# Kernel optimization log

Hardware: AMD Instinct MI355X
Metric: run time of the kernel (lower is better)

## Reference

```python
import jax, jax.numpy as jnp
import numpy as np

B = 1; H = 192; W = 192; DIM = 128; HEADS = 8
WS = 16                      # window_size
OWS = 24                     # overlap_win_size = int(16*0.5)+16
PAD = 4                      # (OWS-WS)//2
C2 = DIM // 2                # per-branch channels
H2 = HEADS // 2              # per-branch heads
HID = 256                    # mlp_ratio * dim
TBL = (WS + OWS - 1) ** 2    # 1521 rel-pos table entries
SCALE = (C2 // H2) ** (-0.5) # head_dim ** -0.5


def layer_norm(x, w, b, eps=1e-5):
    mu = jnp.mean(x, -1, keepdims=True)
    var = jnp.mean((x - mu) ** 2, -1, keepdims=True)
    return (x - mu) * jax.lax.rsqrt(var + eps) * w + b


def window_partition(x, ws):
    b, h, w, c = x.shape
    x = x.reshape(b, h // ws, ws, w // ws, ws, c).transpose(0, 1, 3, 2, 4, 5)
    return x.reshape(-1, ws, ws, c)


def window_reverse(win, ws, h, w):
    b = win.shape[0] // ((h // ws) * (w // ws))
    x = win.reshape(b, h // ws, w // ws, ws, ws, -1).transpose(0, 1, 3, 2, 4, 5)
    return x.reshape(b, h, w, -1)


def _patch_idx(h, w):
    ri = (jnp.arange(h // WS) * WS)[:, None] + jnp.arange(OWS)  # (nwh, OWS)
    ci = (jnp.arange(w // WS) * WS)[:, None] + jnp.arange(OWS)  # (nww, OWS)
    return ri, ci


def unfold_patches(x):
    # x: (b, h, w, c) -> (b*nw, OWS*OWS, c); matches nn.Unfold(OWS, stride=WS, pad=PAD)
    b, h, w, c = x.shape
    xp = jnp.pad(x, ((0, 0), (PAD, PAD), (PAD, PAD), (0, 0)))
    ri, ci = _patch_idx(h, w)
    p = xp[:, ri[:, None, :, None], ci[None, :, None, :], :]  # (b,nwh,nww,OWS,OWS,c)
    return p.reshape(-1, OWS * OWS, c)


def fold_patches(p, b, h, w):
    # inverse of unfold: scatter-add overlapping patches into (b, h+2PAD, w+2PAD, c)
    nwh, nww = h // WS, w // WS
    c = p.shape[-1]
    p = p.reshape(b, nwh, nww, OWS, OWS, c)
    ri, ci = _patch_idx(h, w)
    canvas = jnp.zeros((b, h + 2 * PAD, w + 2 * PAD, c), p.dtype)
    return canvas.at[:, ri[:, None, :, None], ci[None, :, None, :], :].add(p)


def cubic_kernel(x, A=-0.75):
    # PyTorch bicubic (cubic convolution, A=-0.75)
    ax = jnp.abs(x)
    w1 = ((A + 2.0) * ax - (A + 3.0)) * ax * ax + 1.0
    w2 = A * (ax * (ax * (ax - 5.0) + 8.0) - 4.0)
    return jnp.where(ax <= 1.0, w1, jnp.where(ax < 2.0, w2, 0.0))


def resize_matrix(n_out, n_in):
    # dense 1-D bicubic resize matrix, align_corners=False, border-clamped (torch semantics)
    i = jnp.arange(n_out, dtype=jnp.float32)
    src = (i + 0.5) * (float(n_in) / float(n_out)) - 0.5
    fl = jnp.floor(src)
    idx = fl[:, None] + jnp.arange(-1, 3, dtype=jnp.float32)[None, :]  # (n_out, 4)
    wts = cubic_kernel(src[:, None] - idx)
    idx_c = jnp.clip(idx, 0, n_in - 1).astype(jnp.int32)
    M = jnp.zeros((n_out, n_in), jnp.float32)
    return M.at[jnp.arange(n_out)[:, None], idx_c].add(wts)


def cross_attn(xq, xkv, rpi, wq, wkv, rpb):
    b_, nq, d = xq.shape
    n = xkv.shape[1]
    q = (xq @ wq).reshape(b_, nq, H2, -1).transpose(0, 2, 1, 3)
    k, v = jnp.split(xkv @ wkv, 2, axis=-1)
    k = k.reshape(b_, n, H2, -1).transpose(0, 2, 1, 3)
    v = v.reshape(b_, n, H2, -1).transpose(0, 2, 1, 3)
    attn = jnp.einsum('bhqd,bhkd->bhqk', q * SCALE, k)
    bias = rpb[rpi.reshape(-1)].reshape(WS * WS, OWS * OWS, H2)
    bias = bias.transpose(2, 0, 1) if nq < n else bias.transpose(2, 1, 0)
    attn = jax.nn.softmax(attn + bias[None], axis=-1)
    out = jnp.einsum('bhqk,bhkd->bhqd', attn, v)
    return out.transpose(0, 2, 1, 3).reshape(b_, nq, d)


def gsfn(x, h, w, fc1_w, fc1_b, sgn_w, sgn_b, conv_w, conv_b, fc2_w, fc2_b):
    x = x @ fc1_w + fc1_b  # NOTE: source GSFN never applies self.act
    x1, x2 = jnp.split(x, 2, axis=-1)
    Bn, N, Ch = x2.shape
    x2 = layer_norm(x2, sgn_w, sgn_b).transpose(0, 2, 1).reshape(Bn, Ch, h, w)
    x2 = jax.lax.conv_general_dilated(
        x2, conv_w, (1, 1), ((1, 1), (1, 1)),
        feature_group_count=Ch, dimension_numbers=('NCHW', 'OIHW', 'NCHW'))
    x2 = x2 + conv_b[None, :, None, None]
    x2 = x2.reshape(Bn, Ch, N).transpose(0, 2, 1)
    return (x1 * x2) @ fc2_w + fc2_b


def mstb(x_tkn, ln1_w, ln1_b, q1_w, kv1_w, rpb1, q2_w, kv2_w, rpb2,
         proj_w, proj_b, ln2_w, ln2_b, fc1_w, fc1_b, sgn_w, sgn_b,
         conv_w, conv_b, fc2_w, fc2_b, rpi, h, w):
    b, _, c = x_tkn.shape
    short = x_tkn
    x = layer_norm(x_tkn, ln1_w, ln1_b).reshape(b, h, w, c)
    xw = window_partition(x, WS).reshape(-1, WS * WS, c)     # (b*nw, ws*ws, c)
    xa, xb = jnp.split(xw, 2, axis=-1)
    xb_img = window_reverse(xb.reshape(-1, WS, WS, C2), WS, h, w)  # (b,h,w,C2)
    xb_p = unfold_patches(xb_img)                            # (b*nw, OWS*OWS, C2)
    a = cross_attn(xa, xb_p, rpi, q1_w, kv1_w, rpb1) + xa
    bb = cross_attn(xb_p, xa, rpi, q2_w, kv2_w, rpb2) + xb_p
    folded = fold_patches(bb, b, h, w)                       # (b, h+2p, w+2p, C2)
    Mh = resize_matrix(h, h + 2 * PAD)
    Mw = resize_matrix(w, w + 2 * PAD)
    resized = jnp.einsum('oi,bijc,pj->bopc', Mh, folded, Mw)  # bicubic to (h,w)
    xb2 = window_partition(resized, WS).reshape(-1, WS * WS, C2)
    x = jnp.concatenate([a, xb2], -1)
    x = window_reverse(x.reshape(-1, WS, WS, c), WS, h, w).reshape(b, h * w, c)
    x = x @ proj_w + proj_b + short
    x = gsfn(layer_norm(x, ln2_w, ln2_b), h, w, fc1_w, fc1_b,
             sgn_w, sgn_b, conv_w, conv_b, fc2_w, fc2_b) + x
    return x


def setup_inputs() -> dict:
    key = jax.random.key(0)
    ks = jax.random.split(key, 12)
    rn = lambda k, s, sc: jax.random.normal(k, s, jnp.float32) * sc
    return {
        'x_tkn': jax.random.normal(ks[0], (B, H * W, DIM), jnp.float32),
        'ln1_w': jnp.ones((DIM,), jnp.float32), 'ln1_b': jnp.zeros((DIM,), jnp.float32),
        'q1_w': rn(ks[1], (C2, C2), 0.05), 'kv1_w': rn(ks[2], (C2, 2 * C2), 0.05),
        'rpb1': rn(ks[3], (TBL, H2), 0.02),
        'q2_w': rn(ks[4], (C2, C2), 0.05), 'kv2_w': rn(ks[5], (C2, 2 * C2), 0.05),
        'rpb2': rn(ks[6], (TBL, H2), 0.02),
        'proj_w': rn(ks[7], (DIM, DIM), 0.05), 'proj_b': jnp.zeros((DIM,), jnp.float32),
        'ln2_w': jnp.ones((DIM,), jnp.float32), 'ln2_b': jnp.zeros((DIM,), jnp.float32),
        'fc1_w': rn(ks[8], (DIM, HID), 0.05), 'fc1_b': jnp.zeros((HID,), jnp.float32),
        'sgn_w': jnp.ones((HID // 2,), jnp.float32), 'sgn_b': jnp.zeros((HID // 2,), jnp.float32),
        'conv_w': rn(ks[9], (HID // 2, 1, 3, 3), 0.1), 'conv_b': jnp.zeros((HID // 2,), jnp.float32),
        'fc2_w': rn(ks[10], (HID // 2, DIM), 0.05), 'fc2_b': jnp.zeros((DIM,), jnp.float32),
        'rpi': jax.random.randint(ks[11], (WS * WS, OWS * OWS), 0, TBL),
        'h': H, 'w': W,
    }


def reference(x_tkn, ln1_w, ln1_b, q1_w, kv1_w, rpb1, q2_w, kv2_w, rpb2,
              proj_w, proj_b, ln2_w, ln2_b, fc1_w, fc1_b, sgn_w, sgn_b,
              conv_w, conv_b, fc2_w, fc2_b, rpi, h, w):
    return mstb(x_tkn, ln1_w, ln1_b, q1_w, kv1_w, rpb1, q2_w, kv2_w, rpb2,
                proj_w, proj_b, ln2_w, ln2_b, fc1_w, fc1_b, sgn_w, sgn_b,
                conv_w, conv_b, fc2_w, fc2_b, rpi, h, w)
```

## Files before the change

kernel.cpp:

```cpp
#include <hip/hip_runtime.h>
#include <hip/hip_bf16.h>

#define HH 192
#define WW 192
#define NWIN 12
#define WSZ 16
#define OWSZ 24
#define PADK 4
#define NQ1 256
#define NKV1 576
#define C2K 64
#define H2K 4
#define HD 16
#define NTOK (HH*WW)
#define LOG2E 1.4426950408889634f
#define QSCALE (0.25f * LOG2E)

typedef __hip_bfloat16 bf16;
typedef __attribute__((ext_vector_type(8))) short bf16x8;
typedef __attribute__((ext_vector_type(4))) float f32x4;

union B8 { short s[8]; bf16x8 v; unsigned u[4]; };

__device__ __forceinline__ unsigned cvtpk(float lo, float hi)
{
    unsigned r;
    asm("v_cvt_pk_bf16_f32 %0, %1, %2" : "=v"(r) : "v"(lo), "v"(hi));
    return r;
}

__launch_bounds__(256)
__global__ void ln_kernel(const float* __restrict__ in, int is, int io,
                          float* __restrict__ out, int os, int oo,
                          const float* __restrict__ g, const float* __restrict__ b,
                          int M)
{
    int row = blockIdx.x * 4 + (threadIdx.x >> 6);
    if (row >= M) return;
    int lane = threadIdx.x & 63;
    const float* p = in + (size_t)row * is + io;
    float v0 = p[lane * 2], v1 = p[lane * 2 + 1];
    float s = v0 + v1, sq = v0 * v0 + v1 * v1;
#pragma unroll
    for (int o = 32; o > 0; o >>= 1) { s += __shfl_xor(s, o); sq += __shfl_xor(sq, o); }
    float mu  = s * 0.0078125f;
    float var = sq * 0.0078125f - mu * mu;
    float inv = 1.0f / sqrtf(var + 1e-5f);
    float* q = out + (size_t)row * os + oo;
    q[lane * 2]     = (v0 - mu) * inv * g[lane * 2]     + b[lane * 2];
    q[lane * 2 + 1] = (v1 - mu) * inv * g[lane * 2 + 1] + b[lane * 2 + 1];
}

__global__ void wcombT_kernel(const float* __restrict__ q1_w, const float* __restrict__ kv1_w,
                              const float* __restrict__ q2_w, const float* __restrict__ kv2_w,
                              bf16* __restrict__ WT)
{
    int idx = blockIdx.x * 256 + threadIdx.x;
    if (idx >= 384 * 128) return;
    int c = idx >> 7, r = idx & 127;
    float v = 0.f;
    if (c < 64)       { if (r < 64)  v = q1_w[r * 64 + c] * QSCALE; }
    else if (c < 192) { if (r >= 64) v = kv1_w[(r - 64) * 128 + (c - 64)]; }
    else if (c < 256) { if (r >= 64) v = q2_w[(r - 64) * 64 + (c - 192)] * QSCALE; }
    else              { if (r < 64)  v = kv2_w[r * 128 + (c - 256)]; }
    WT[idx] = __float2bfloat16(v);
}

__global__ void wtrans_kernel(const float* __restrict__ src, int N, bf16* __restrict__ dst)
{
// ... 5 lines not shown

__global__ void bias1_kernel(const float* __restrict__ rpb1, const int* __restrict__ rpi,
                             float* __restrict__ biasT)
{
    int idx = blockIdx.x * 256 + threadIdx.x;
    if (idx >= H2K * NKV1 * NQ1) return;
    int q = idx & 255;
    int n = (idx >> 8) % NKV1;
    int h = idx / (NKV1 * NQ1);
    biasT[idx] = rpb1[rpi[q * NKV1 + n] * H2K + h] * LOG2E;
}

__global__ void bias2_kernel(const float* __restrict__ rpb2, const int* __restrict__ rpi,
                             float* __restrict__ biasT)
{
    int idx = blockIdx.x * 256 + threadIdx.x;
    if (idx >= H2K * NQ1 * NKV1) return;
    int q = idx % NKV1;
    int k = (idx / NKV1) % NQ1;
    int h = idx / (NKV1 * NQ1);
    biasT[idx] = rpb2[rpi[k * NKV1 + q] * H2K + h] * LOG2E;
}

__launch_bounds__(256)
__global__ void attn1_mfma(const unsigned* __restrict__ qkvu,
                           const float* __restrict__ lnx,
                           const float* __restrict__ biasT,
                           float* __restrict__ xcat)
{
    __shared__ unsigned K_lds[NKV1][10];
    __shared__ unsigned V_lds[NKV1][10];

    const int win = blockIdx.x, h = blockIdx.y;
    const int wi = win / NWIN, wj = win % NWIN;
    const int tid = threadIdx.x;
    const int lane = tid & 63, w = tid >> 6;
    const int g = lane >> 4, qloc = lane & 15;

    for (int n = tid; n < NKV1; n += 256) {
        int rr = wi * WSZ - PADK + n / OWSZ, cc = wj * WSZ - PADK + n % OWSZ;
        bool ib = (rr >= 0 && rr < HH && cc >= 0 && cc < WW);
        uint4 k0v = make_uint4(0, 0, 0, 0), k1v = k0v, v0v = k0v, v1v = k0v;
        if (ib) {
            const unsigned* src = qkvu + (size_t)(rr * WW + cc) * 96 + 32 + 8 * h;
            k0v = *(const uint4*)(src);
            k1v = *(const uint4*)(src + 4);
            v0v = *(const uint4*)(src + 32);
            v1v = *(const uint4*)(src + 36);
        }
        *(uint4*)&K_lds[n][0] = k0v; *(uint4*)&K_lds[n][4] = k1v;
        *(uint4*)&V_lds[n][0] = v0v; *(uint4*)&V_lds[n][4] = v1v;
    }
    __syncthreads();

    const int q0base = blockIdx.z * 128 + w * 32;
    bf16x8 qfrag[2];
#pragma unroll
    for (int qt = 0; qt < 2; qt++) {
        int q = q0base + qt * 16 + qloc;
        int pix = (wi * WSZ + (q >> 4)) * WW + wj * WSZ + (q & 15);
        B8 f;
#pragma unroll
        for (int j = 0; j < 4; j++) f.u[j] = 0;
        if (g < 2)
            f.v = *(const bf16x8*)(qkvu + (size_t)pix * 96 + 8 * h + 4 * g);
        qfrag[qt] = f.v;
    }

    f32x4 O[2];
    float lsum[2];
#pragma unroll
    for (int qt = 0; qt < 2; qt++) { O[qt] = (f32x4){0.f, 0.f, 0.f, 0.f}; lsum[qt] = 0.f; }
    const f32x4 zz = {0.f, 0.f, 0.f, 0.f};

    for (int step = 0; step < 18; step++) {
        const int k0 = step * 32;
        bf16x8 kfA, kfB;
        if (g < 2) {
            kfA = *(const bf16x8*)&K_lds[k0 + qloc][4 * g];
            kfB = *(const bf16x8*)&K_lds[k0 + 16 + qloc][4 * g];
        } else {
            B8 zf;
#pragma unroll
            for (int j = 0; j < 4; j++) zf.u[j] = 0;
            kfA = zf.v; kfB = zf.v;
        }
        B8 vf;
#pragma unroll
        for (int j = 0; j < 8; j++) {
            int key = k0 + 4 * g + (j & 3) + ((j >> 2) << 4);
            unsigned word = V_lds[key][qloc >> 1];
            vf.s[j] = (short)((qloc & 1) ? (word >> 16) : (word & 0xffff));
        }

#pragma unroll
        for (int qt = 0; qt < 2; qt++) {
            f32x4 sA = __builtin_amdgcn_mfma_f32_16x16x32_bf16(kfA, qfrag[qt], zz, 0, 0, 0);
            f32x4 sB = __builtin_amdgcn_mfma_f32_16x16x32_bf16(kfB, qfrag[qt], zz, 0, 0, 0);
            int qa = q0base + qt * 16 + qloc;
            const float* bpA = biasT + ((size_t)h * NKV1 + k0 + 4 * g) * NQ1 + qa;
            const float* bpB = bpA + 16 * NQ1;
            float pa[4], pb[4];
            float ls = 0.f;
#pragma unroll
            for (int r = 0; r < 4; r++) {
                pa[r] = exp2f(sA[r] + bpA[(size_t)r * NQ1]);
                pb[r] = exp2f(sB[r] + bpB[(size_t)r * NQ1]);
                ls += pa[r] + pb[r];
            }
            B8 pf;
            pf.u[0] = cvtpk(pa[0], pa[1]);
            pf.u[1] = cvtpk(pa[2], pa[3]);
            pf.u[2] = cvtpk(pb[0], pb[1]);
            pf.u[3] = cvtpk(pb[2], pb[3]);
            lsum[qt] += ls;
            O[qt] = __builtin_amdgcn_mfma_f32_16x16x32_bf16(vf.v, pf.v, O[qt], 0, 0, 0);
        }
    }

#pragma unroll
    for (int qt = 0; qt < 2; qt++) {
        float lt = lsum[qt];
        lt += __shfl_xor(lt, 16);
        lt += __shfl_xor(lt, 32);
        float rl = 1.f / lt;
        int q = q0base + qt * 16 + qloc;
        int pix = (wi * WSZ + (q >> 4)) * WW + wj * WSZ + (q & 15);
        size_t base = (size_t)pix * 128 + h * HD + 4 * g;
#pragma unroll
        for (int r = 0; r < 4; r++)
            xcat[base + r] = O[qt][r] * rl + lnx[base + r];
    }
}

__launch_bounds__(256)
__global__ void attn2_mfma(const unsigned* __restrict__ qkvu,
                           const float* __restrict__ lnx,
                           const float* __restrict__ biasT,
                           float* __restrict__ bb)
{
    __shared__ unsigned K_lds[NQ1][10];
    __shared__ unsigned V_lds[NQ1][10];

    const int win = blockIdx.x, h = blockIdx.y;
    const int wi = win / NWIN, wj = win % NWIN;
    const int tid = threadIdx.x;
    const int lane = tid & 63, w = tid >> 6;
    const int g = lane >> 4, qloc = lane & 15;

    {
        int n = tid;
        int pix = (wi * WSZ + (n >> 4)) * WW + wj * WSZ + (n & 15);
        const unsigned* src = qkvu + (size_t)pix * 96 + 32 + 8 * h;
        *(uint4*)&K_lds[n][0] = *(const uint4*)(src);
        *(uint4*)&K_lds[n][4] = *(const uint4*)(src + 4);
        *(uint4*)&V_lds[n][0] = *(const uint4*)(src + 32);
        *(uint4*)&V_lds[n][4] = *(const uint4*)(src + 36);
    }
    __syncthreads();

    const int q0base = blockIdx.z * 192 + w * 48;
    bf16x8 qfrag[3];
    bool qin[3];
    int qpix[3];
#pragma unroll
    for (int qt = 0; qt < 3; qt++) {
        int qa = q0base + qt * 16 + qloc;
        int gr = wi * WSZ - PADK + qa / OWSZ, gc = wj * WSZ - PADK + qa % OWSZ;
        bool ib = (gr >= 0 && gr < HH && gc >= 0 && gc < WW);
        qin[qt] = ib;
        qpix[qt] = ib ? gr * WW + gc : 0;
        B8 f;
#pragma unroll
        for (int j = 0; j < 4; j++) f.u[j] = 0;
        if (ib && g < 2)
            f.v = *(const bf16x8*)(qkvu + (size_t)qpix[qt] * 96 + 8 * h + 4 * g);
        qfrag[qt] = f.v;
    }

    f32x4 O[3];
    float lsum[3];
#pragma unroll
    for (int qt = 0; qt < 3; qt++) { O[qt] = (f32x4){0.f, 0.f, 0.f, 0.f}; lsum[qt] = 0.f; }
    const f32x4 zz = {0.f, 0.f, 0.f, 0.f};

    for (int step = 0; step < 8; step++) {
        const int k0 = step * 32;
        bf16x8 kfA, kfB;
        if (g < 2) {
            kfA = *(const bf16x8*)&K_lds[k0 + qloc][4 * g];
            kfB = *(const bf16x8*)&K_lds[k0 + 16 + qloc][4 * g];
        } else {
            B8 zf;
#pragma unroll
            for (int j = 0; j < 4; j++) zf.u[j] = 0;
            kfA = zf.v; kfB = zf.v;
        }
        B8 vf;
#pragma unroll
        for (int j = 0; j < 8; j++) {
            int key = k0 + 4 * g + (j & 3) + ((j >> 2) << 4);
            unsigned word = V_lds[key][qloc >> 1];
            vf.s[j] = (short)((qloc & 1) ? (word >> 16) : (word & 0xffff));
        }

#pragma unroll
        for (int qt = 0; qt < 3; qt++) {
            f32x4 sA = __builtin_amdgcn_mfma_f32_16x16x32_bf16(kfA, qfrag[qt], zz, 0, 0, 0);
            f32x4 sB = __builtin_amdgcn_mfma_f32_16x16x32_bf16(kfB, qfrag[qt], zz, 0, 0, 0);
            int qa = q0base + qt * 16 + qloc;
            const float* bpA = biasT + ((size_t)h * NQ1 + k0 + 4 * g) * NKV1 + qa;
            const float* bpB = bpA + 16 * NKV1;
            float pa[4], pb[4];
            float ls = 0.f;
#pragma unroll
            for (int r = 0; r < 4; r++) {
                pa[r] = exp2f(sA[r] + bpA[(size_t)r * NKV1]);
                pb[r] = exp2f(sB[r] + bpB[(size_t)r * NKV1]);
                ls += pa[r] + pb[r];
            }
            B8 pf;
            pf.u[0] = cvtpk(pa[0], pa[1]);
            pf.u[1] = cvtpk(pa[2], pa[3]);
            pf.u[2] = cvtpk(pb[0], pb[1]);
            pf.u[3] = cvtpk(pb[2], pb[3]);
            lsum[qt] += ls;
            O[qt] = __builtin_amdgcn_mfma_f32_16x16x32_bf16(vf.v, pf.v, O[qt], 0, 0, 0);
        }
    }

#pragma unroll
    for (int qt = 0; qt < 3; qt++) {
        float lt = lsum[qt];
        lt += __shfl_xor(lt, 16);
        lt += __shfl_xor(lt, 32);
        float rl = 1.f / lt;
        int qa = q0base + qt * 16 + qloc;
        size_t obase = ((size_t)win * NKV1 + qa) * C2K + h * HD + 4 * g;
        size_t rbase = (size_t)qpix[qt] * 128 + C2K + h * HD + 4 * g;
#pragma unroll
        for (int r = 0; r < 4; r++)
            bb[obase + r] = O[qt][r] * rl + (qin[qt] ? lnx[rbase + r] : 0.f);
    }
}

__global__ void fold_kernel(const float* __restrict__ bb, float* __restrict__ folded)
{
    int idx = blockIdx.x * 256 + threadIdx.x;
    if (idx >= 200 * 200 * 64) return;
    int c = idx & 63;
    int j = (idx >> 6) % 200;
    int i = idx / (64 * 200);
    int ilo = (i > 23) ? ((i - 8) >> 4) : 0;
    int ihi = min(11, i >> 4);
    int jlo = (j > 23) ? ((j - 8) >> 4) : 0;
    int jhi = min(11, j >> 4);
    float s = 0.f;
    for (int wi = ilo; wi <= ihi; wi++)
        for (int wj = jlo; wj <= jhi; wj++) {
            int p = (i - wi * 16) * OWSZ + (j - wj * 16);
            s += bb[((size_t)(wi * NWIN + wj) * NKV1 + p) * C2K + c];
        }
    folded[idx] = s;
}

__device__ __forceinline__ float cubicw(float x)
{
    float ax = fabsf(x);
    const float A = -0.75f;
    if (ax <= 1.f) return ((A + 2.f) * ax - (A + 3.f)) * ax * ax + 1.f;
    if (ax < 2.f)  return A * (ax * (ax * (ax - 5.f) + 8.f) - 4.f);
    return 0.f;
}

__global__ void resize_kernel(const float* __restrict__ folded, float* __restrict__ xcat)
{
    int idx = blockIdx.x * 256 + threadIdx.x;
    if (idx >= HH * WW * C2K) return;
    int c = idx & 63;
    int p = (idx >> 6) % WW;
    int o = idx / (C2K * WW);
    const float ratio = 200.f / 192.f;
    float sr = (o + 0.5f) * ratio - 0.5f;
    float sc = (p + 0.5f) * ratio - 0.5f;
    int fr = (int)floorf(sr), fcc = (int)floorf(sc);
    float wc[4]; int ic[4];
#pragma unroll
    for (int u = 0; u < 4; u++) {
        int jj = fcc - 1 + u;
        wc[u] = cubicw(sc - (float)jj);
        ic[u] = min(max(jj, 0), 199);
    }
    float acc = 0.f;
#pragma unroll
    for (int t = 0; t < 4; t++) {
        int ii = fr - 1 + t;
        float wr = cubicw(sr - (float)ii);
        int ir = min(max(ii, 0), 199);
        const float* rowp = folded + ((size_t)ir * 200) * 64 + c;
        float rs = 0.f;
#pragma unroll
        for (int u = 0; u < 4; u++) rs += wc[u] * rowp[(size_t)ic[u] * 64];
        acc += wr * rs;
    }
    xcat[(size_t)(o * WW + p) * 128 + C2K + c] = acc;
}

template<int NTPW, bool OBF>
__launch_bounds__(256)
__global__ void gemm_mfma(const float* __restrict__ A1, int a1s,
                          const float* __restrict__ A2, int a2s,
                          const bf16* __restrict__ WT,
                          const float* __restrict__ bias,
                          const float* __restrict__ R, int rs,
                          float* __restrict__ C, int cs)
{
    const int tid = threadIdx.x;
    const int lane = tid & 63, w = tid >> 6;
    const int g = lane >> 4, nl = lane & 15;

    bf16x8 wf[NTPW][4];
#pragma unroll
    for (int t = 0; t < NTPW; t++) {
        int ncol = (w * NTPW + t) * 16 + nl;
        const bf16* wp = WT + (size_t)ncol * 128;
#pragma unroll
        for (int ks = 0; ks < 4; ks++)
            wf[t][ks] = *(const bf16x8*)(wp + ks * 32 + 8 * g);
    }

    const f32x4 zz = {0.f, 0.f, 0.f, 0.f};
    const int row = (blockIdx.x * 4 + blockIdx.y) * 16 + nl;

    bf16x8 xf[4];
    const float* ap = A1 + (size_t)row * a1s + 8 * g;
#pragma unroll
    for (int ks = 0; ks < 4; ks++) {
        float4 v0 = *(const float4*)(ap + ks * 32);
        float4 v1 = *(const float4*)(ap + ks * 32 + 4);
        if (A2) {
            const float* ap2 = A2 + (size_t)row * a2s + 8 * g + ks * 32;
            float4 m0 = *(const float4*)(ap2);
            float4 m1 = *(const float4*)(ap2 + 4);
            v0.x *= m0.x; v0.y *= m0.y; v0.z *= m0.z; v0.w *= m0.w;
            v1.x *= m1.x; v1.y *= m1.y; v1.z *= m1.z; v1.w *= m1.w;
        }
        B8 f;
        f.u[0] = cvtpk(v0.x, v0.y);
// ... 13 lines not shown
            acc[t] = __builtin_amdgcn_mfma_f32_16x16x32_bf16(wf[t][ks], xf[ks], acc[t], 0, 0, 0);

#pragma unroll
    for (int t = 0; t < NTPW; t++) {
        const int n0t = (w * NTPW + t) * 16 + 4 * g;
        if (OBF) {
            unsigned* Cu = (unsigned*)C + (size_t)row * (cs >> 1) + (n0t >> 1);
            uint2 o;
            o.x = cvtpk(acc[t][0], acc[t][1]);
            o.y = cvtpk(acc[t][2], acc[t][3]);
            *(uint2*)Cu = o;
        } else {
            float4 o;
            o.x = acc[t][0]; o.y = acc[t][1]; o.z = acc[t][2]; o.w = acc[t][3];
            if (bias) {
                float4 bv = *(const float4*)(bias + n0t);
                o.x += bv.x; o.y += bv.y; o.z += bv.z; o.w += bv.w;
            }
            if (R) {
                float4 rv = *(const float4*)(R + (size_t)row * rs + n0t);
                o.x += rv.x; o.y += rv.y; o.z += rv.z; o.w += rv.w;
            }
            *(float4*)(C + (size_t)row * cs + n0t) = o;
        }
    }
}

__global__ void dwconv_kernel(const float* __restrict__ x2n,
                              const float* __restrict__ conv_w,
                              const float* __restrict__ conv_b,
                              float* __restrict__ x2c)
{
    int idx = blockIdx.x * 256 + threadIdx.x;
    if (idx >= NTOK * 128) return;
    int ch = idx & 127, t = idx >> 7;
    int i = t / WW, j = t % WW;
    float acc = conv_b[ch];
#pragma unroll
    for (int a = 0; a < 3; a++) {
        int ii = i + a - 1;
        if (ii < 0 || ii >= HH) continue;
#pragma unroll
        for (int b = 0; b < 3; b++) {
            int jj = j + b - 1;
            if (jj < 0 || jj >= WW) continue;
            acc += conv_w[ch * 9 + a * 3 + b] * x2n[(size_t)(ii * WW + jj) * 256 + ch];
// ... 24 lines not shown
    const float* fc1_b  = (const float*)d_in[14];
    const float* sgn_w  = (const float*)d_in[15];
    const float* sgn_b  = (const float*)d_in[16];
    const float* conv_w = (const float*)d_in[17];
    const float* conv_b = (const float*)d_in[18];
    const float* fc2_w  = (const float*)d_in[19];
    const float* fc2_b  = (const float*)d_in[20];
    const int*   rpi    = (const int*)d_in[21];

    float* ws = (float*)d_ws;
    float* lnx    = ws;
    float* xcat   = ws + 4718592;
    float* bbuf   = ws + 9437184;
    bf16*  projT  = (bf16*)(ws + 14155776);
    bf16*  fc1T   = (bf16*)(ws + 14163968);
    bf16*  fc2T   = (bf16*)(ws + 14180352);
    float* bias1T = ws + 14745600;
    float* bias2T = ws + 17104896;
    float* qkv    = ws + 17694720;
    bf16*  wcombT = (bf16*)(ws + 21233664);
    float* foldp  = ws + 17694720;
    float* h1     = ws + 14745600;
    float* out    = (float*)d_out;

    ln_kernel<<<NTOK / 4, 256, 0, stream>>>(x_tkn, 128, 0, lnx, 128, 0, ln1_w, ln1_b, NTOK);
    wcombT_kernel<<<(384 * 128) / 256, 256, 0, stream>>>(q1_w, kv1_w, q2_w, kv2_w, wcombT);
    bias1_kernel<<<(H2K * NKV1 * NQ1) / 256, 256, 0, stream>>>(rpb1, rpi, bias1T);
    bias2_kernel<<<(H2K * NQ1 * NKV1) / 256, 256, 0, stream>>>(rpb2, rpi, bias2T);
    gemm_mfma<3, true><<<dim3(NTOK / 64, 4), 256, 0, stream>>>(lnx, 128, nullptr, 0, wcombT,
                                                               nullptr, nullptr, 0, qkv, 192);
    attn1_mfma<<<dim3(144, 4, 2), 256, 0, stream>>>((const unsigned*)qkv, lnx, bias1T, xcat);
    gemm_mfma<3, true><<<dim3(NTOK / 64, 4), 256, 0, stream>>>(lnx, 128, nullptr, 0,
                                                               wcombT + 192 * 128,
                                                               nullptr, nullptr, 0, qkv, 192);
    attn2_mfma<<<dim3(144, 4, 3), 256, 0, stream>>>((const unsigned*)qkv, lnx, bias2T, bbuf);
    fold_kernel<<<(200 * 200 * 64) / 256, 256, 0, stream>>>(bbuf, foldp);
    wtrans_kernel<<<(128 * 128) / 256, 256, 0, stream>>>(proj_w, 128, projT);
    wtrans_kernel<<<(256 * 128) / 256, 256, 0, stream>>>(fc1_w, 256, fc1T);
    wtrans_kernel<<<(128 * 128) / 256, 256, 0, stream>>>(fc2_w, 128, fc2T);
    resize_kernel<<<(HH * WW * C2K) / 256, 256, 0, stream>>>(foldp, xcat);
    gemm_mfma<2, false><<<dim3(NTOK / 64, 4), 256, 0, stream>>>(xcat, 128, nullptr, 0, projT,
                                                                proj_b, x_tkn, 128, lnx, 128);
    ln_kernel<<<NTOK / 4, 256, 0, stream>>>(lnx, 128, 0, bbuf, 128, 0, ln2_w, ln2_b, NTOK);
    gemm_mfma<4, false><<<dim3(NTOK / 64, 4), 256, 0, stream>>>(bbuf, 128, nullptr, 0, fc1T,
                                                                fc1_b, nullptr, 0, h1, 256);
    ln_kernel<<<NTOK / 4, 256, 0, stream>>>(h1, 256, 128, h1, 256, 128, sgn_w, sgn_b, NTOK);
    dwconv_kernel<<<(NTOK * 128) / 256, 256, 0, stream>>>(h1 + 128, conv_w, conv_b, xcat);
    gemm_mfma<2, false><<<dim3(NTOK / 64, 4), 256, 0, stream>>>(h1, 256, xcat, 128, fc2T,
                                                                fc2_b, lnx, 128, out, 128);
}
```

Measured before the change: 323.3 us.

## Fuse LayerNorm2 into proj GEMM and SG-norm into fc1 GEMM epilogues

After: 305.1 us. 5.6% less time.

```diff
diff --git a/kernel.cpp b/kernel.cpp
--- a/kernel.cpp
+++ b/kernel.cpp
@@ -44,7 +44,7 @@
 #pragma unroll
     for (int o = 32; o > 0; o >>= 1) { s += __shfl_xor(s, o); sq += __shfl_xor(sq, o); }
     float mu  = s * 0.0078125f;
-    float var = sq * 0.0078125f - mu * mu;
+    float var = fmaxf(sq * 0.0078125f - mu * mu, 0.f);
     float inv = 1.0f / sqrtf(var + 1e-5f);
     float* q = out + (size_t)row * os + oo;
     q[lane * 2]     = (v0 - mu) * inv * g[lane * 2]     + b[lane * 2];
@@ -96,290 +96,6 @@
     biasT[idx] = rpb2[rpi[k * NKV1 + q] * H2K + h] * LOG2E;
 }
 
-__launch_bounds__(256)
-__global__ void attn1_mfma(const unsigned* __restrict__ qkvu,
-                           const float* __restrict__ lnx,
-                           const float* __restrict__ biasT,
-                           float* __restrict__ xcat)
-{
-    __shared__ unsigned K_lds[NKV1][10];
-    __shared__ unsigned V_lds[NKV1][10];
-
-    const int win = blockIdx.x, h = blockIdx.y;
-    const int wi = win / NWIN, wj = win % NWIN;
-    const int tid = threadIdx.x;
-    const int lane = tid & 63, w = tid >> 6;
-    const int g = lane >> 4, qloc = lane & 15;
-
-    for (int n = tid; n < NKV1; n += 256) {
-        int rr = wi * WSZ - PADK + n / OWSZ, cc = wj * WSZ - PADK + n % OWSZ;
-        bool ib = (rr >= 0 && rr < HH && cc >= 0 && cc < WW);
-        uint4 k0v = make_uint4(0, 0, 0, 0), k1v = k0v, v0v = k0v, v1v = k0v;
-        if (ib) {
-            const unsigned* src = qkvu + (size_t)(rr * WW + cc) * 96 + 32 + 8 * h;
-            k0v = *(const uint4*)(src);
-            k1v = *(const uint4*)(src + 4);
-            v0v = *(const uint4*)(src + 32);
-            v1v = *(const uint4*)(src + 36);
-        }
-        *(uint4*)&K_lds[n][0] = k0v; *(uint4*)&K_lds[n][4] = k1v;
-        *(uint4*)&V_lds[n][0] = v0v; *(uint4*)&V_lds[n][4] = v1v;
-    }
-    __syncthreads();
-
-    const int q0base = blockIdx.z * 128 + w * 32;
-    bf16x8 qfrag[2];
-#pragma unroll
-    for (int qt = 0; qt < 2; qt++) {
-        int q = q0base + qt * 16 + qloc;
-        int pix = (wi * WSZ + (q >> 4)) * WW + wj * WSZ + (q & 15);
-        B8 f;
-#pragma unroll
-        for (int j = 0; j < 4; j++) f.u[j] = 0;
-        if (g < 2)
-            f.v = *(const bf16x8*)(qkvu + (size_t)pix * 96 + 8 * h + 4 * g);
-        qfrag[qt] = f.v;
-    }
-
-    f32x4 O[2];
-    float lsum[2];
-#pragma unroll
-    for (int qt = 0; qt < 2; qt++) { O[qt] = (f32x4){0.f, 0.f, 0.f, 0.f}; lsum[qt] = 0.f; }
-    const f32x4 zz = {0.f, 0.f, 0.f, 0.f};
-
-    for (int step = 0; step < 18; step++) {
-        const int k0 = step * 32;
-        bf16x8 kfA, kfB;
-        if (g < 2) {
-            kfA = *(const bf16x8*)&K_lds[k0 + qloc][4 * g];
-            kfB = *(const bf16x8*)&K_lds[k0 + 16 + qloc][4 * g];
-        } else {
-            B8 zf;
-#pragma unroll
-            for (int j = 0; j < 4; j++) zf.u[j] = 0;
-            kfA = zf.v; kfB = zf.v;
-        }
-        B8 vf;
-#pragma unroll
-        for (int j = 0; j < 8; j++) {
-            int key = k0 + 4 * g + (j & 3) + ((j >> 2) << 4);
-            unsigned word = V_lds[key][qloc >> 1];
-            vf.s[j] = (short)((qloc & 1) ? (word >> 16) : (word & 0xffff));
-        }
-
-#pragma unroll
-        for (int qt = 0; qt < 2; qt++) {
-            f32x4 sA = __builtin_amdgcn_mfma_f32_16x16x32_bf16(kfA, qfrag[qt], zz, 0, 0, 0);
-            f32x4 sB = __builtin_amdgcn_mfma_f32_16x16x32_bf16(kfB, qfrag[qt], zz, 0, 0, 0);
-            int qa = q0base + qt * 16 + qloc;
-            const float* bpA = biasT + ((size_t)h * NKV1 + k0 + 4 * g) * NQ1 + qa;
-            const float* bpB = bpA + 16 * NQ1;
-            float pa[4], pb[4];
-            float ls = 0.f;
-#pragma unroll
-            for (int r = 0; r < 4; r++) {
-                pa[r] = exp2f(sA[r] + bpA[(size_t)r * NQ1]);
-                pb[r] = exp2f(sB[r] + bpB[(size_t)r * NQ1]);
-                ls += pa[r] + pb[r];
-            }
-            B8 pf;
-            pf.u[0] = cvtpk(pa[0], pa[1]);
-            pf.u[1] = cvtpk(pa[2], pa[3]);
-            pf.u[2] = cvtpk(pb[0], pb[1]);
-            pf.u[3] = cvtpk(pb[2], pb[3]);
-            lsum[qt] += ls;
-            O[qt] = __builtin_amdgcn_mfma_f32_16x16x32_bf16(vf.v, pf.v, O[qt], 0, 0, 0);
-        }
-    }
-
-#pragma unroll
-    for (int qt = 0; qt < 2; qt++) {
-        float lt = lsum[qt];
-        lt += __shfl_xor(lt, 16);
-        lt += __shfl_xor(lt, 32);
-        float rl = 1.f / lt;
-        int q = q0base + qt * 16 + qloc;
-        int pix = (wi * WSZ + (q >> 4)) * WW + wj * WSZ + (q & 15);
-        size_t base = (size_t)pix * 128 + h * HD + 4 * g;
-#pragma unroll
-        for (int r = 0; r < 4; r++)
-            xcat[base + r] = O[qt][r] * rl + lnx[base + r];
-    }
-}
-
-__launch_bounds__(256)
-__global__ void attn2_mfma(const unsigned* __restrict__ qkvu,
-                           const float* __restrict__ lnx,
-                           const float* __restrict__ biasT,
-                           float* __restrict__ bb)
-{
-    __shared__ unsigned K_lds[NQ1][10];
-    __shared__ unsigned V_lds[NQ1][10];
-
-    const int win = blockIdx.x, h = blockIdx.y;
-    const int wi = win / NWIN, wj = win % NWIN;
-    const int tid = threadIdx.x;
-    const int lane = tid & 63, w = tid >> 6;
-    const int g = lane >> 4, qloc = lane & 15;
-
-    {
-        int n = tid;
-        int pix = (wi * WSZ + (n >> 4)) * WW + wj * WSZ + (n & 15);
-        const unsigned* src = qkvu + (size_t)pix * 96 + 32 + 8 * h;
-        *(uint4*)&K_lds[n][0] = *(const uint4*)(src);
-        *(uint4*)&K_lds[n][4] = *(const uint4*)(src + 4);
-        *(uint4*)&V_lds[n][0] = *(const uint4*)(src + 32);
-        *(uint4*)&V_lds[n][4] = *(const uint4*)(src + 36);
-    }
-    __syncthreads();
-
-    const int q0base = blockIdx.z * 192 + w * 48;
-    bf16x8 qfrag[3];
-    bool qin[3];
-    int qpix[3];
-#pragma unroll
-    for (int qt = 0; qt < 3; qt++) {
-        int qa = q0base + qt * 16 + qloc;
-        int gr = wi * WSZ - PADK + qa / OWSZ, gc = wj * WSZ - PADK + qa % OWSZ;
-        bool ib = (gr >= 0 && gr < HH && gc >= 0 && gc < WW);
-        qin[qt] = ib;
-        qpix[qt] = ib ? gr * WW + gc : 0;
-        B8 f;
-#pragma unroll
-        for (int j = 0; j < 4; j++) f.u[j] = 0;
-        if (ib && g < 2)
-            f.v = *(const bf16x8*)(qkvu + (size_t)qpix[qt] * 96 + 8 * h + 4 * g);
-        qfrag[qt] = f.v;
-    }
-
-    f32x4 O[3];
-    float lsum[3];
-#pragma unroll
-    for (int qt = 0; qt < 3; qt++) { O[qt] = (f32x4){0.f, 0.f, 0.f, 0.f}; lsum[qt] = 0.f; }
-    const f32x4 zz = {0.f, 0.f, 0.f, 0.f};
-
-    for (int step = 0; step < 8; step++) {
-        const int k0 = step * 32;
-        bf16x8 kfA, kfB;
-        if (g < 2) {
-            kfA = *(const bf16x8*)&K_lds[k0 + qloc][4 * g];
-            kfB = *(const bf16x8*)&K_lds[k0 + 16 + qloc][4 * g];
-        } else {
-            B8 zf;
-#pragma unroll
-            for (int j = 0; j < 4; j++) zf.u[j] = 0;
-            kfA = zf.v; kfB = zf.v;
-        }
-        B8 vf;
-#pragma unroll
-        for (int j = 0; j < 8; j++) {
-            int key = k0 + 4 * g + (j & 3) + ((j >> 2) << 4);
-            unsigned word = V_lds[key][qloc >> 1];
-            vf.s[j] = (short)((qloc & 1) ? (word >> 16) : (word & 0xffff));
-        }
-
-#pragma unroll
-        for (int qt = 0; qt < 3; qt++) {
-            f32x4 sA = __builtin_amdgcn_mfma_f32_16x16x32_bf16(kfA, qfrag[qt], zz, 0, 0, 0);
-            f32x4 sB = __builtin_amdgcn_mfma_f32_16x16x32_bf16(kfB, qfrag[qt], zz, 0, 0, 0);
-            int qa = q0base + qt * 16 + qloc;
-            const float* bpA = biasT + ((size_t)h * NQ1 + k0 + 4 * g) * NKV1 + qa;
-            const float* bpB = bpA + 16 * NKV1;
-            float pa[4], pb[4];
-            float ls = 0.f;
-#pragma unroll
-            for (int r = 0; r < 4; r++) {
-                pa[r] = exp2f(sA[r] + bpA[(size_t)r * NKV1]);
-                pb[r] = exp2f(sB[r] + bpB[(size_t)r * NKV1]);
-                ls += pa[r] + pb[r];
-            }
-            B8 pf;
-            pf.u[0] = cvtpk(pa[0], pa[1]);
-            pf.u[1] = cvtpk(pa[2], pa[3]);
-            pf.u[2] = cvtpk(pb[0], pb[1]);
-            pf.u[3] = cvtpk(pb[2], pb[3]);
-            lsum[qt] += ls;
-            O[qt] = __builtin_amdgcn_mfma_f32_16x16x32_bf16(vf.v, pf.v, O[qt], 0, 0, 0);
-        }
-    }
-
-#pragma unroll
-    for (int qt = 0; qt < 3; qt++) {
-        float lt = lsum[qt];
-        lt += __shfl_xor(lt, 16);
-        lt += __shfl_xor(lt, 32);
-        float rl = 1.f / lt;
-        int qa = q0base + qt * 16 + qloc;
-        size_t obase = ((size_t)win * NKV1 + qa) * C2K + h * HD + 4 * g;
-        size_t rbase = (size_t)qpix[qt] * 128 + C2K + h * HD + 4 * g;
-#pragma unroll
-        for (int r = 0; r < 4; r++)
-            bb[obase + r] = O[qt][r] * rl + (qin[qt] ? lnx[rbase + r] : 0.f);
-    }
-}
-
-__global__ void fold_kernel(const float* __restrict__ bb, float* __restrict__ folded)
-{
-    int idx = blockIdx.x * 256 + threadIdx.x;
-    if (idx >= 200 * 200 * 64) return;
-    int c = idx & 63;
-    int j = (idx >> 6) % 200;
-    int i = idx / (64 * 200);
-    int ilo = (i > 23) ? ((i - 8) >> 4) : 0;
-    int ihi = min(11, i >> 4);
-    int jlo = (j > 23) ? ((j - 8) >> 4) : 0;
-    int jhi = min(11, j >> 4);
-    float s = 0.f;
-    for (int wi = ilo; wi <= ihi; wi++)
-        for (int wj = jlo; wj <= jhi; wj++) {
-            int p = (i - wi * 16) * OWSZ + (j - wj * 16);
-            s += bb[((size_t)(wi * NWIN + wj) * NKV1 + p) * C2K + c];
-        }
-    folded[idx] = s;
-}
-
-__device__ __forceinline__ float cubicw(float x)
-{
-    float ax = fabsf(x);
-    const float A = -0.75f;
-    if (ax <= 1.f) return ((A + 2.f) * ax - (A + 3.f)) * ax * ax + 1.f;
-    if (ax < 2.f)  return A * (ax * (ax * (ax - 5.f) + 8.f) - 4.f);
-    return 0.f;
-}
-
-__global__ void resize_kernel(const float* __restrict__ folded, float* __restrict__ xcat)
-{
-    int idx = blockIdx.x * 256 + threadIdx.x;
-    if (idx >= HH * WW * C2K) return;
-    int c = idx & 63;
-    int p = (idx >> 6) % WW;
-    int o = idx / (C2K * WW);
-    const float ratio = 200.f / 192.f;
-    float sr = (o + 0.5f) * ratio - 0.5f;
-    float sc = (p + 0.5f) * ratio - 0.5f;
-    int fr = (int)floorf(sr), fcc = (int)floorf(sc);
-    float wc[4]; int ic[4];
-#pragma unroll
-    for (int u = 0; u < 4; u++) {
-        int jj = fcc - 1 + u;
-        wc[u] = cubicw(sc - (float)jj);
-        ic[u] = min(max(jj, 0), 199);
-    }
-    float acc = 0.f;
-#pragma unroll
-    for (int t = 0; t < 4; t++) {
-        int ii = fr - 1 + t;
-        float wr = cubicw(sr - (float)ii);
-        int ir = min(max(ii, 0), 199);
-        const float* rowp = folded + ((size_t)ir * 200) * 64 + c;
-        float rs = 0.f;
-#pragma unroll
-        for (int u = 0; u < 4; u++) rs += wc[u] * rowp[(size_t)ic[u] * 64];
-        acc += wr * rs;
-    }
-    xcat[(size_t)(o * WW + p) * 128 + C2K + c] = acc;
-}
-
 template<int NTPW, bool OBF>
 __launch_bounds__(256)
 __global__ void gemm_mfma(const float* __restrict__ A1, int a1s,
@@ -396,8 +112,7 @@
     bf16x8 wf[NTPW][4];
 #pragma unroll
     for (int t = 0; t < NTPW; t++) {
-        int ncol = (w * NTPW + t) * 16 + nl;
-        const bf16* wp = WT + (size_t)ncol * 128;
+        const bf16* wp = WT + (size_t)((w * NTPW + t) * 16 + nl) * 128;
 #pragma unroll
         for (int ks = 0; ks < 4; ks++)
             wf[t][ks] = *(const bf16x8*)(wp + ks * 32 + 8 * g);
@@ -457,6 +172,480 @@
                 o.x += rv.x; o.y += rv.y; o.z += rv.z; o.w += rv.w;
             }
             *(float4*)(C + (size_t)row * cs + n0t) = o;
+        }
+    }
+}
+
+__launch_bounds__(256)
+__global__ void attn1_mfma(const unsigned* __restrict__ qkvu,
+                           const float* __restrict__ lnx,
+                           const float* __restrict__ biasT,
+                           float* __restrict__ xcat)
+{
+    __shared__ unsigned K_lds[NKV1][10];
+    __shared__ unsigned V_lds[NKV1][10];
+
+    const int win = blockIdx.x, h = blockIdx.y;
+    const int wi = win / NWIN, wj = win % NWIN;
+    const int tid = threadIdx.x;
+    const int lane = tid & 63, w = tid >> 6;
+    const int g = lane >> 4, qloc = lane & 15;
+
+    for (int n = tid; n < NKV1; n += 256) {
+        int rr = wi * WSZ - PADK + n / OWSZ, cc = wj * WSZ - PADK + n % OWSZ;
+        bool ib = (rr >= 0 && rr < HH && cc >= 0 && cc < WW);
+        uint4 k0v = make_uint4(0, 0, 0, 0), k1v = k0v, v0v = k0v, v1v = k0v;
+        if (ib) {
+            const unsigned* src = qkvu + (size_t)(rr * WW + cc) * 96 + 32 + 8 * h;
+            k0v = *(const uint4*)(src);
+            k1v = *(const uint4*)(src + 4);
+            v0v = *(const uint4*)(src + 32);
+            v1v = *(const uint4*)(src + 36);
+        }
+        *(uint4*)&K_lds[n][0] = k0v; *(uint4*)&K_lds[n][4] = k1v;
+        *(uint4*)&V_lds[n][0] = v0v; *(uint4*)&V_lds[n][4] = v1v;
+    }
+    __syncthreads();
+
+    const int q0base = blockIdx.z * 128 + w * 32;
+    bf16x8 qfrag[2];
+#pragma unroll
+    for (int qt = 0; qt < 2; qt++) {
+        int q = q0base + qt * 16 + qloc;
+        int pix = (wi * WSZ + (q >> 4)) * WW + wj * WSZ + (q & 15);
+        B8 f;
+#pragma unroll
+        for (int j = 0; j < 4; j++) f.u[j] = 0;
+        if (g < 2)
+            f.v = *(const bf16x8*)(qkvu + (size_t)pix * 96 + 8 * h + 4 * g);
+        qfrag[qt] = f.v;
+    }
+
+    f32x4 O[2];
+    float lsum[2];
+#pragma unroll
+    for (int qt = 0; qt < 2; qt++) { O[qt] = (f32x4){0.f, 0.f, 0.f, 0.f}; lsum[qt] = 0.f; }
+    const f32x4 zz = {0.f, 0.f, 0.f, 0.f};
+
+    for (int step = 0; step < 18; step++) {
+        const int k0 = step * 32;
+        bf16x8 kfA, kfB;
+        if (g < 2) {
+            kfA = *(const bf16x8*)&K_lds[k0 + qloc][4 * g];
+            kfB = *(const bf16x8*)&K_lds[k0 + 16 + qloc][4 * g];
+        } else {
+            B8 zf;
+#pragma unroll
+            for (int j = 0; j < 4; j++) zf.u[j] = 0;
+            kfA = zf.v; kfB = zf.v;
+        }
+        B8 vf;
+#pragma unroll
+        for (int j = 0; j < 8; j++) {
+            int key = k0 + 4 * g + (j & 3) + ((j >> 2) << 4);
+            unsigned word = V_lds[key][qloc >> 1];
+            vf.s[j] = (short)((qloc & 1) ? (word >> 16) : (word & 0xffff));
+        }
+
+#pragma unroll
+        for (int qt = 0; qt < 2; qt++) {
+            f32x4 sA = __builtin_amdgcn_mfma_f32_16x16x32_bf16(kfA, qfrag[qt], zz, 0, 0, 0);
+            f32x4 sB = __builtin_amdgcn_mfma_f32_16x16x32_bf16(kfB, qfrag[qt], zz, 0, 0, 0);
+            int qa = q0base + qt * 16 + qloc;
+            const float* bpA = biasT + ((size_t)h * NKV1 + k0 + 4 * g) * NQ1 + qa;
+            const float* bpB = bpA + 16 * NQ1;
+            float pa[4], pb[4];
+            float ls = 0.f;
+#pragma unroll
+            for (int r = 0; r < 4; r++) {
+                pa[r] = exp2f(sA[r] + bpA[(size_t)r * NQ1]);
+                pb[r] = exp2f(sB[r] + bpB[(size_t)r * NQ1]);
+                ls += pa[r] + pb[r];
+            }
+            B8 pf;
+            pf.u[0] = cvtpk(pa[0], pa[1]);
+            pf.u[1] = cvtpk(pa[2], pa[3]);
+            pf.u[2] = cvtpk(pb[0], pb[1]);
+            pf.u[3] = cvtpk(pb[2], pb[3]);
+            lsum[qt] += ls;
+            O[qt] = __builtin_amdgcn_mfma_f32_16x16x32_bf16(vf.v, pf.v, O[qt], 0, 0, 0);
+        }
+    }
+
+#pragma unroll
+    for (int qt = 0; qt < 2; qt++) {
+        float lt = lsum[qt];
+        lt += __shfl_xor(lt, 16);
+        lt += __shfl_xor(lt, 32);
+        float rl = 1.f / lt;
+        int q = q0base + qt * 16 + qloc;
+        int pix = (wi * WSZ + (q >> 4)) * WW + wj * WSZ + (q & 15);
+        size_t base = (size_t)pix * 128 + h * HD + 4 * g;
+#pragma unroll
+        for (int r = 0; r < 4; r++)
+            xcat[base + r] = O[qt][r] * rl + lnx[base + r];
+    }
+}
+
+__launch_bounds__(256)
+__global__ void attn2_mfma(const unsigned* __restrict__ qkvu,
+                           const float* __restrict__ lnx,
+                           const float* __restrict__ biasT,
+                           float* __restrict__ bb)
+{
+    __shared__ unsigned K_lds[NQ1][10];
+    __shared__ unsigned V_lds[NQ1][10];
+
+    const int win = blockIdx.x, h = blockIdx.y;
+    const int wi = win / NWIN, wj = win % NWIN;
+    const int tid = threadIdx.x;
+    const int lane = tid & 63, w = tid >> 6;
+    const int g = lane >> 4, qloc = lane & 15;
+
+    {
+        int n = tid;
+        int pix = (wi * WSZ + (n >> 4)) * WW + wj * WSZ + (n & 15);
+        const unsigned* src = qkvu + (size_t)pix * 96 + 32 + 8 * h;
+        *(uint4*)&K_lds[n][0] = *(const uint4*)(src);
+        *(uint4*)&K_lds[n][4] = *(const uint4*)(src + 4);
+        *(uint4*)&V_lds[n][0] = *(const uint4*)(src + 32);
+        *(uint4*)&V_lds[n][4] = *(const uint4*)(src + 36);
+    }
+    __syncthreads();
+
+    const int q0base = blockIdx.z * 192 + w * 48;
+    bf16x8 qfrag[3];
+    bool qin[3];
+    int qpix[3];
+#pragma unroll
+    for (int qt = 0; qt < 3; qt++) {
+        int qa = q0base + qt * 16 + qloc;
+        int gr = wi * WSZ - PADK + qa / OWSZ, gc = wj * WSZ - PADK + qa % OWSZ;
+        bool ib = (gr >= 0 && gr < HH && gc >= 0 && gc < WW);
+        qin[qt] = ib;
+        qpix[qt] = ib ? gr * WW + gc : 0;
+        B8 f;
+#pragma unroll
+        for (int j = 0; j < 4; j++) f.u[j] = 0;
+        if (ib && g < 2)
+            f.v = *(const bf16x8*)(qkvu + (size_t)qpix[qt] * 96 + 8 * h + 4 * g);
+        qfrag[qt] = f.v;
+    }
+
+    f32x4 O[3];
+    float lsum[3];
+#pragma unroll
+    for (int qt = 0; qt < 3; qt++) { O[qt] = (f32x4){0.f, 0.f, 0.f, 0.f}; lsum[qt] = 0.f; }
+    const f32x4 zz = {0.f, 0.f, 0.f, 0.f};
+
+    for (int step = 0; step < 8; step++) {
+        const int k0 = step * 32;
+        bf16x8 kfA, kfB;
+        if (g < 2) {
+            kfA = *(const bf16x8*)&K_lds[k0 + qloc][4 * g];
+            kfB = *(const bf16x8*)&K_lds[k0 + 16 + qloc][4 * g];
+        } else {
+            B8 zf;
+#pragma unroll
+            for (int j = 0; j < 4; j++) zf.u[j] = 0;
+            kfA = zf.v; kfB = zf.v;
+        }
+        B8 vf;
+#pragma unroll
+        for (int j = 0; j < 8; j++) {
+            int key = k0 + 4 * g + (j & 3) + ((j >> 2) << 4);
+            unsigned word = V_lds[key][qloc >> 1];
+            vf.s[j] = (short)((qloc & 1) ? (word >> 16) : (word & 0xffff));
+        }
+
+#pragma unroll
+        for (int qt = 0; qt < 3; qt++) {
+            f32x4 sA = __builtin_amdgcn_mfma_f32_16x16x32_bf16(kfA, qfrag[qt], zz, 0, 0, 0);
+            f32x4 sB = __builtin_amdgcn_mfma_f32_16x16x32_bf16(kfB, qfrag[qt], zz, 0, 0, 0);
+            int qa = q0base + qt * 16 + qloc;
+            const float* bpA = biasT + ((size_t)h * NQ1 + k0 + 4 * g) * NKV1 + qa;
+            const float* bpB = bpA + 16 * NKV1;
+            float pa[4], pb[4];
+            float ls = 0.f;
+#pragma unroll
+            for (int r = 0; r < 4; r++) {
+                pa[r] = exp2f(sA[r] + bpA[(size_t)r * NKV1]);
+                pb[r] = exp2f(sB[r] + bpB[(size_t)r * NKV1]);
+                ls += pa[r] + pb[r];
+            }
+            B8 pf;
+            pf.u[0] = cvtpk(pa[0], pa[1]);
+            pf.u[1] = cvtpk(pa[2], pa[3]);
+            pf.u[2] = cvtpk(pb[0], pb[1]);
+            pf.u[3] = cvtpk(pb[2], pb[3]);
+            lsum[qt] += ls;
+            O[qt] = __builtin_amdgcn_mfma_f32_16x16x32_bf16(vf.v, pf.v, O[qt], 0, 0, 0);
+        }
+    }
+
+#pragma unroll
+    for (int qt = 0; qt < 3; qt++) {
+        float lt = lsum[qt];
+        lt += __shfl_xor(lt, 16);
+        lt += __shfl_xor(lt, 32);
+        float rl = 1.f / lt;
+        int qa = q0base + qt * 16 + qloc;
+        size_t obase = ((size_t)win * NKV1 + qa) * C2K + h * HD + 4 * g;
+        size_t rbase = (size_t)qpix[qt] * 128 + C2K + h * HD + 4 * g;
+#pragma unroll
+        for (int r = 0; r < 4; r++)
+            bb[obase + r] = O[qt][r] * rl + (qin[qt] ? lnx[rbase + r] : 0.f);
+    }
+}
+
+__global__ void fold_kernel(const float* __restrict__ bb, float* __restrict__ folded)
+{
+    int idx = blockIdx.x * 256 + threadIdx.x;
+    if (idx >= 200 * 200 * 64) return;
+    int c = idx & 63;
+    int j = (idx >> 6) % 200;
+    int i = idx / (64 * 200);
+    int ilo = (i > 23) ? ((i - 8) >> 4) : 0;
+    int ihi = min(11, i >> 4);
+    int jlo = (j > 23) ? ((j - 8) >> 4) : 0;
+    int jhi = min(11, j >> 4);
+    float s = 0.f;
+    for (int wi = ilo; wi <= ihi; wi++)
+        for (int wj = jlo; wj <= jhi; wj++) {
+            int p = (i - wi * 16) * OWSZ + (j - wj * 16);
+            s += bb[((size_t)(wi * NWIN + wj) * NKV1 + p) * C2K + c];
+        }
+    folded[idx] = s;
+}
+
+__device__ __forceinline__ float cubicw(float x)
+{
+    float ax = fabsf(x);
+    const float A = -0.75f;
+    if (ax <= 1.f) return ((A + 2.f) * ax - (A + 3.f)) * ax * ax + 1.f;
+    if (ax < 2.f)  return A * (ax * (ax * (ax - 5.f) + 8.f) - 4.f);
+    return 0.f;
+}
+
+__global__ void resize_kernel(const float* __restrict__ folded, float* __restrict__ xcat)
+{
+    int idx = blockIdx.x * 256 + threadIdx.x;
+    if (idx >= HH * WW * C2K) return;
+    int c = idx & 63;
+    int p = (idx >> 6) % WW;
+    int o = idx / (C2K * WW);
+    const float ratio = 200.f / 192.f;
+    float sr = (o + 0.5f) * ratio - 0.5f;
+    float sc = (p + 0.5f) * ratio - 0.5f;
+    int fr = (int)floorf(sr), fcc = (int)floorf(sc);
+    float wc[4]; int ic[4];
+#pragma unroll
+    for (int u = 0; u < 4; u++) {
+        int jj = fcc - 1 + u;
+        wc[u] = cubicw(sc - (float)jj);
+        ic[u] = min(max(jj, 0), 199);
+    }
+    float acc = 0.f;
+#pragma unroll
+    for (int t = 0; t < 4; t++) {
+        int ii = fr - 1 + t;
+        float wr = cubicw(sr - (float)ii);
+        int ir = min(max(ii, 0), 199);
+        const float* rowp = folded + ((size_t)ir * 200) * 64 + c;
+        float rs = 0.f;
+#pragma unroll
+        for (int u = 0; u < 4; u++) rs += wc[u] * rowp[(size_t)ic[u] * 64];
+        acc += wr * rs;
+    }
+    xcat[(size_t)(o * WW + p) * 128 + C2K + c] = acc;
+}
+
+__launch_bounds__(256)
+__global__ void proj_ln2(const float* __restrict__ A1,
+                         const bf16* __restrict__ WT,
+                         const float* __restrict__ bias,
+                         const float* __restrict__ R,
+                         const float* __restrict__ ln2w, const float* __restrict__ ln2b,
+                         float* __restrict__ xbuf, unsigned* __restrict__ ybf)
+{
+    __shared__ float psum[16][16];
+    __shared__ float psq[16][16];
+    __shared__ float mu_s[16], inv_s[16];
+
+    const int tid = threadIdx.x;
+    const int lane = tid & 63, w = tid >> 6;
+    const int g = lane >> 4, nl = lane & 15;
+
+    bf16x8 wf[2][4];
+#pragma unroll
+    for (int t = 0; t < 2; t++) {
+        const bf16* wp = WT + (size_t)((w * 2 + t) * 16 + nl) * 128;
+#pragma unroll
+        for (int ks = 0; ks < 4; ks++)
+            wf[t][ks] = *(const bf16x8*)(wp + ks * 32 + 8 * g);
+    }
+
+    const int row = (blockIdx.x * 4 + blockIdx.y) * 16 + nl;
+    bf16x8 xf[4];
+    const float* ap = A1 + (size_t)row * 128 + 8 * g;
+#pragma unroll
+    for (int ks = 0; ks < 4; ks++) {
+        float4 v0 = *(const float4*)(ap + ks * 32);
+        float4 v1 = *(const float4*)(ap + ks * 32 + 4);
+        B8 f;
+        f.u[0] = cvtpk(v0.x, v0.y);
+        f.u[1] = cvtpk(v0.z, v0.w);
+        f.u[2] = cvtpk(v1.x, v1.y);
+        f.u[3] = cvtpk(v1.z, v1.w);
+        xf[ks] = f.v;
+    }
+
+    const f32x4 zz = {0.f, 0.f, 0.f, 0.f};
+    f32x4 acc[2];
+    acc[0] = zz; acc[1] = zz;
+#pragma unroll
+    for (int ks = 0; ks < 4; ks++) {
+        acc[0] = __builtin_amdgcn_mfma_f32_16x16x32_bf16(wf[0][ks], xf[ks], acc[0], 0, 0, 0);
+        acc[1] = __builtin_amdgcn_mfma_f32_16x16x32_bf16(wf[1][ks], xf[ks], acc[1], 0, 0, 0);
+    }
+
+    float o[2][4];
+    float s = 0.f, sq = 0.f;
+#pragma unroll
+    for (int t = 0; t < 2; t++) {
+        int n0t = (w * 2 + t) * 16 + 4 * g;
+        float4 bv = *(const float4*)(bias + n0t);
+        float4 rv = *(const float4*)(R + (size_t)row * 128 + n0t);
+        o[t][0] = acc[t][0] + bv.x + rv.x;
+        o[t][1] = acc[t][1] + bv.y + rv.y;
+        o[t][2] = acc[t][2] + bv.z + rv.z;
+        o[t][3] = acc[t][3] + bv.w + rv.w;
+#pragma unroll
+        for (int r = 0; r < 4; r++) { s += o[t][r]; sq += o[t][r] * o[t][r]; }
+    }
+    psum[nl][w * 4 + g] = s;
+    psq[nl][w * 4 + g] = sq;
+    __syncthreads();
+    if (tid < 16) {
+        float ts = 0.f, tq = 0.f;
+#pragma unroll
+        for (int i = 0; i < 16; i++) { ts += psum[tid][i]; tq += psq[tid][i]; }
+        float mu = ts * 0.0078125f;
+        float var = fmaxf(tq * 0.0078125f - mu * mu, 0.f);
+        mu_s[tid] = mu;
+        inv_s[tid] = 1.0f / sqrtf(var + 1e-5f);
+    }
+    __syncthreads();
+
+    float mu = mu_s[nl], inv = inv_s[nl];
+#pragma unroll
+    for (int t = 0; t < 2; t++) {
+        int n0t = (w * 2 + t) * 16 + 4 * g;
+        *(float4*)(xbuf + (size_t)row * 128 + n0t) = make_float4(o[t][0], o[t][1], o[t][2], o[t][3]);
+        float4 gw = *(const float4*)(ln2w + n0t);
+        float4 gb = *(const float4*)(ln2b + n0t);
+        float y0 = (o[t][0] - mu) * inv * gw.x + gb.x;
+        float y1 = (o[t][1] - mu) * inv * gw.y + gb.y;
+        float y2 = (o[t][2] - mu) * inv * gw.z + gb.z;
+        float y3 = (o[t][3] - mu) * inv * gw.w + gb.w;
+        uint2 yo;
+        yo.x = cvtpk(y0, y1);
+        yo.y = cvtpk(y2, y3);
+        *(uint2*)(ybf + (size_t)row * 64 + (n0t >> 1)) = yo;
+    }
+}
+
+__launch_bounds__(256)
+__global__ void fc1_sgn(const unsigned* __restrict__ ybf,
+                        const bf16* __restrict__ WT,
+                        const float* __restrict__ bias,
+                        const float* __restrict__ sgnw, const float* __restrict__ sgnb,
+                        float* __restrict__ h1)
+{
+    __shared__ float psum[16][8];
+    __shared__ float psq[16][8];
+    __shared__ float mu_s[16], inv_s[16];
+
+    const int tid = threadIdx.x;
+    const int lane = tid & 63, w = tid >> 6;
+    const int g = lane >> 4, nl = lane & 15;
+
+    bf16x8 wf[4][4];
+#pragma unroll
+    for (int t = 0; t < 4; t++) {
+        const bf16* wp = WT + (size_t)((w * 4 + t) * 16 + nl) * 128;
+#pragma unroll
+        for (int ks = 0; ks < 4; ks++)
+            wf[t][ks] = *(const bf16x8*)(wp + ks * 32 + 8 * g);
+    }
+
+    const int row = (blockIdx.x * 4 + blockIdx.y) * 16 + nl;
+    bf16x8 xf[4];
+    const unsigned* ap = ybf + (size_t)row * 64 + 4 * g;
+#pragma unroll
+    for (int ks = 0; ks < 4; ks++)
+        xf[ks] = *(const bf16x8*)(ap + ks * 16);
+
+    const f32x4 zz = {0.f, 0.f, 0.f, 0.f};
+    f32x4 acc[4];
+#pragma unroll
+    for (int t = 0; t < 4; t++) acc[t] = zz;
+#pragma unroll
+    for (int ks = 0; ks < 4; ks++)
+#pragma unroll
+        for (int t = 0; t < 4; t++)
+            acc[t] = __builtin_amdgcn_mfma_f32_16x16x32_bf16(wf[t][ks], xf[ks], acc[t], 0, 0, 0);
+
+    float o[4][4];
+    float s = 0.f, sq = 0.f;
+#pragma unroll
+    for (int t = 0; t < 4; t++) {
+        int n0t = (w * 4 + t) * 16 + 4 * g;
+        float4 bv = *(const float4*)(bias + n0t);
+        o[t][0] = acc[t][0] + bv.x;
+        o[t][1] = acc[t][1] + bv.y;
+        o[t][2] = acc[t][2] + bv.z;
+        o[t][3] = acc[t][3] + bv.w;
+    }
+    if (w >= 2) {
+#pragma unroll
+        for (int t = 0; t < 4; t++)
+#pragma unroll
+            for (int r = 0; r < 4; r++) { s += o[t][r]; sq += o[t][r] * o[t][r]; }
+        psum[nl][(w - 2) * 4 + g] = s;
+        psq[nl][(w - 2) * 4 + g] = sq;
+    }
+    __syncthreads();
+    if (tid < 16) {
+        float ts = 0.f, tq = 0.f;
+#pragma unroll
+        for (int i = 0; i < 8; i++) { ts += psum[tid][i]; tq += psq[tid][i]; }
+        float mu = ts * 0.0078125f;
+        float var = fmaxf(tq * 0.0078125f - mu * mu, 0.f);
+        mu_s[tid] = mu;
+        inv_s[tid] = 1.0f / sqrtf(var + 1e-5f);
+    }
+    __syncthreads();
+
+    if (w < 2) {
+#pragma unroll
+        for (int t = 0; t < 4; t++) {
+            int n0t = (w * 4 + t) * 16 + 4 * g;
+            *(float4*)(h1 + (size_t)row * 256 + n0t) = make_float4(o[t][0], o[t][1], o[t][2], o[t][3]);
+        }
+    } else {
+        float mu = mu_s[nl], inv = inv_s[nl];
+#pragma unroll
+        for (int t = 0; t < 4; t++) {
+            int n0t = (w * 4 + t) * 16 + 4 * g;
+            float4 gw = *(const float4*)(sgnw + n0t - 128);
+            float4 gb = *(const float4*)(sgnb + n0t - 128);
+            float4 y;
+            y.x = (o[t][0] - mu) * inv * gw.x + gb.x;
+            y.y = (o[t][1] - mu) * inv * gw.y + gb.y;
+            y.z = (o[t][2] - mu) * inv * gw.z + gb.z;
+            y.w = (o[t][3] - mu) * inv * gw.w + gb.w;
+            *(float4*)(h1 + (size_t)row * 256 + n0t) = y;
         }
     }
 }
@@ -527,6 +716,7 @@
     float* foldp  = ws + 17694720;
     float* h1     = ws + 14745600;
     float* out    = (float*)d_out;
+    unsigned* ybf = (unsigned*)bbuf;
 
     ln_kernel<<<NTOK / 4, 256, 0, stream>>>(x_tkn, 128, 0, lnx, 128, 0, ln1_w, ln1_b, NTOK);
     wcombT_kernel<<<(384 * 128) / 256, 256, 0, stream>>>(q1_w, kv1_w, q2_w, kv2_w, wcombT);
@@ -544,12 +734,9 @@
     wtrans_kernel<<<(256 * 128) / 256, 256, 0, stream>>>(fc1_w, 256, fc1T);
     wtrans_kernel<<<(128 * 128) / 256, 256, 0, stream>>>(fc2_w, 128, fc2T);
     resize_kernel<<<(HH * WW * C2K) / 256, 256, 0, stream>>>(foldp, xcat);
-    gemm_mfma<2, false><<<dim3(NTOK / 64, 4), 256, 0, stream>>>(xcat, 128, nullptr, 0, projT,
-                                                                proj_b, x_tkn, 128, lnx, 128);
-    ln_kernel<<<NTOK / 4, 256, 0, stream>>>(lnx, 128, 0, bbuf, 128, 0, ln2_w, ln2_b, NTOK);
-    gemm_mfma<4, false><<<dim3(NTOK / 64, 4), 256, 0, stream>>>(bbuf, 128, nullptr, 0, fc1T,
-                                                                fc1_b, nullptr, 0, h1, 256);
-    ln_kernel<<<NTOK / 4, 256, 0, stream>>>(h1, 256, 128, h1, 256, 128, sgn_w, sgn_b, NTOK);
+    proj_ln2<<<dim3(NTOK / 64, 4), 256, 0, stream>>>(xcat, projT, proj_b, x_tkn,
+                                                     ln2_w, ln2_b, lnx, ybf);
+    fc1_sgn<<<dim3(NTOK / 64, 4), 256, 0, stream>>>(ybf, fc1T, fc1_b, sgn_w, sgn_b, h1);
     dwconv_kernel<<<(NTOK * 128) / 256, 256, 0, stream>>>(h1 + 128, conv_w, conv_b, xcat);
     gemm_mfma<2, false><<<dim3(NTOK / 64, 4), 256, 0, stream>>>(h1, 256, xcat, 128, fc2T,
                                                                 fc2_b, lnx, 128, out, 128);
```
